# Kernel tuning notes

Hardware: AMD Instinct MI355X
Metric: run time of the kernel (lower is better)

The kernel has to match this reference:

```python
import jax, jax.numpy as jnp
import numpy as np
from jax import lax

DIM = 512
IDIM = 1536
K = 7


def setup_inputs() -> dict:
    key = jax.random.key(0)
    ks = jax.random.split(key, 10)
    B, C, T = 16, DIM, 2048
    x = jax.random.normal(ks[0], (B, C, T), dtype=jnp.float32)
    dw_w = jax.random.normal(ks[1], (DIM, 1, K), dtype=jnp.float32) * (1.0 / np.sqrt(K))
    dw_b = jax.random.normal(ks[2], (DIM,), dtype=jnp.float32) * 0.01
    ln_g = jnp.ones((DIM,), dtype=jnp.float32)
    ln_b = jnp.zeros((DIM,), dtype=jnp.float32)
    w1 = jax.random.normal(ks[3], (IDIM, DIM), dtype=jnp.float32) * (1.0 / np.sqrt(DIM))
    b1 = jax.random.normal(ks[4], (IDIM,), dtype=jnp.float32) * 0.01
    grn_g = jax.random.normal(ks[5], (IDIM,), dtype=jnp.float32) * 0.02
    grn_b = jax.random.normal(ks[6], (IDIM,), dtype=jnp.float32) * 0.02
    w2 = jax.random.normal(ks[7], (DIM, IDIM), dtype=jnp.float32) * (1.0 / np.sqrt(IDIM))
    b2 = jax.random.normal(ks[8], (DIM,), dtype=jnp.float32) * 0.01
    return {"x": x, "dw_w": dw_w, "dw_b": dw_b, "ln_g": ln_g, "ln_b": ln_b,
            "w1": w1, "b1": b1, "grn_g": grn_g, "grn_b": grn_b, "w2": w2, "b2": b2}


def reference(x, dw_w, dw_b, ln_g, ln_b, w1, b1, grn_g, grn_b, w2, b2):
    residual = x  # [B, C, T]
    # depthwise conv1d, padding='same' style (K//2 each side)
    y = lax.conv_general_dilated(
        x, dw_w,
        window_strides=(1,),
        padding=[(K // 2, K // 2)],
        dimension_numbers=("NCH", "OIH", "NCH"),
        feature_group_count=DIM,
    ) + dw_b[None, :, None]
    y = jnp.transpose(y, (0, 2, 1))  # [B, T, C]
    # LayerNorm over channels, eps=1e-6
    mu = jnp.mean(y, axis=-1, keepdims=True)
    var = jnp.mean((y - mu) ** 2, axis=-1, keepdims=True)
    y = (y - mu) * lax.rsqrt(var + 1e-6) * ln_g + ln_b
    # pwconv1 + GELU (exact, erf-based as torch default)
    h = jnp.einsum("btc,ic->bti", y, w1) + b1  # [B, T, IDIM]
    h = jax.nn.gelu(h, approximate=False)
    # GRN: L2 norm over time axis (dim=1), mean over channels
    gx = jnp.sqrt(jnp.sum(h * h, axis=1, keepdims=True))  # [B, 1, IDIM]
    nx = gx / (jnp.mean(gx, axis=-1, keepdims=True) + 1e-6)
    h = grn_g * (h * nx) + grn_b + h
    # pwconv2
    y = jnp.einsum("bti,ci->btc", h, w2) + b2  # [B, T, C]
    y = jnp.transpose(y, (0, 2, 1))  # [B, C, T]
    return residual + y
```

## Files before the change

kernel.cpp:

```cpp
#include <hip/hip_runtime.h>
#include <math.h>

typedef unsigned short u16;
typedef unsigned int u32;
typedef __bf16 bf16x8_t __attribute__((ext_vector_type(8)));
typedef float f32x4_t __attribute__((ext_vector_type(4)));

__device__ __forceinline__ u16 f2bf(float f) {
  __bf16 b = (__bf16)f;
  return __builtin_bit_cast(u16, b);
}

__device__ __forceinline__ void gld16(const void* g, void* l) {
  __builtin_amdgcn_global_load_lds(
      (const __attribute__((address_space(1))) void*)g,
      (__attribute__((address_space(3))) void*)l, 16, 0, 0);
}

__global__ __launch_bounds__(256) void cast_kernel(const float* __restrict__ src,
                                                   u16* __restrict__ dst, int n) {
  int i = (blockIdx.x * 256 + threadIdx.x) * 4;
  if (i < n) {
    float4 v = *(const float4*)(src + i);
    uint2 o;
    o.x = (u32)f2bf(v.x) | ((u32)f2bf(v.y) << 16);
    o.y = (u32)f2bf(v.z) | ((u32)f2bf(v.w) << 16);
    *(uint2*)(dst + i) = o;
  }
}

__global__ __launch_bounds__(64) void b2ob_kernel(const float* __restrict__ w2,
                                                  const float* __restrict__ grn_b,
                                                  const float* __restrict__ b2,
                                                  float* __restrict__ out) {
  int c = blockIdx.x;
  int l = threadIdx.x;
  float p = 0.f;
  for (int i = l; i < 1536; i += 64) p += grn_b[i] * w2[(size_t)c * 1536 + i];
  #pragma unroll
  for (int s = 32; s; s >>= 1) p += __shfl_xor(p, s);
  if (l == 0) out[c] = b2[c] + p;
}

__global__ __launch_bounds__(512, 4) void conv_ln_kernel(const float* __restrict__ X,
                                                         const float* __restrict__ Wd,
                                                         const float* __restrict__ bd,
                                                         const float* __restrict__ lng,
                                                         const float* __restrict__ lnb,
                                                         u16* __restrict__ Y) {
  __shared__ float ystage[16 * 516];
  __shared__ float mu_s[16], rs_s[16];

  const int c = threadIdx.x;
  const int b = blockIdx.y;
  const int t0 = blockIdx.x * 64;

  const float* xr = X + ((size_t)b * 512 + c) * 2048;
  float wr[7];
  #pragma unroll
  for (int k = 0; k < 7; ++k) wr[k] = Wd[c * 7 + k];
  const float bdv = bd[c];
  const float lg = lng[c];
  const float lb = lnb[c];

  for (int ch = 0; ch < 4; ++ch) {
    const int tc0 = t0 + ch * 16;
    const int g = tc0 - 4;
    float w[24];
    if (g >= 0 && g + 24 <= 2048) {
      #pragma unroll
      for (int q = 0; q < 6; ++q) {
        float4 v = *(const float4*)(xr + g + q * 4);
        w[q * 4 + 0] = v.x; w[q * 4 + 1] = v.y;
        w[q * 4 + 2] = v.z; w[q * 4 + 3] = v.w;
      }
    } else {
      #pragma unroll
      for (int j = 0; j < 24; ++j) {
        int tt = g + j;
        w[j] = (tt >= 0 && tt < 2048) ? xr[tt] : 0.f;
      }
    }
    float outv[16];
    #pragma unroll
    for (int i = 0; i < 16; ++i) {
      float a = bdv;
      #pragma unroll
      for (int k = 0; k < 7; ++k) a = fmaf(w[i + 1 + k], wr[k], a);
      outv[i] = a;
      ystage[i * 516 + c] = a;
    }
    __syncthreads();
    {
      int r = c >> 5, cl = c & 31;
      float s = 0.f, q = 0.f;
      #pragma unroll
      for (int k = 0; k < 16; ++k) {
        float v = ystage[r * 516 + cl + k * 32];
        s += v; q += v * v;
      }
      #pragma unroll
      for (int m = 16; m; m >>= 1) { s += __shfl_xor(s, m); q += __shfl_xor(q, m); }
      if (cl == 0) {
        float mu = s * (1.f / 512.f);
        float var = q * (1.f / 512.f) - mu * mu;
        mu_s[r] = mu;
        rs_s[r] = rsqrtf(var + 1e-6f);
      }
    }
    __syncthreads();
    #pragma unroll
    for (int i = 0; i < 16; ++i) {
      float v = (outv[i] - mu_s[i]) * rs_s[i] * lg + lb;
      Y[(size_t)(b * 2048 + tc0 + i) * 512 + c] = f2bf(v);
    }
  }
}

__global__ __launch_bounds__(256, 2) void gemm1_kernel(const u16* __restrict__ A,
                                                       const u16* __restrict__ B,
                                                       const float* __restrict__ b1,
                                                       u16* __restrict__ H,
                                                       float* __restrict__ gsum) {
  __shared__ __align__(16) u16 smem[128 * 136];
  u16* lA = smem;
  u16* lB = smem + 128 * 64;

  const int tid = threadIdx.x;
  const int w = tid >> 6;
  const int l = tid & 63;
  const int m0 = blockIdx.x * 128;
  const int n0 = blockIdx.y * 128;
  const int bidx = m0 >> 11;
  const int wm = w >> 1, wn = w & 1;

  f32x4_t acc[4][4];
  #pragma unroll
  for (int i = 0; i < 4; ++i)
    #pragma unroll
    for (int j = 0; j < 4; ++j) {
      f32x4_t z = {0.f, 0.f, 0.f, 0.f};
      acc[i][j] = z;
    }

  const int rowInc = w * 8 + (l >> 3);
  const int colE = (l & 7) * 8;
  const u16* Abase = A + (size_t)(m0 + rowInc) * 512 + colE;
  const u16* Bbase = B + (size_t)(n0 + rowInc) * 512 + colE;
  const int ldsOff = w * 512;

  for (int kt = 0; kt < 512; kt += 64) {
    #pragma unroll
    for (int c = 0; c < 4; ++c) {
      gld16(Abase + (size_t)(c * 32) * 512 + kt, lA + c * 2048 + ldsOff);
      gld16(Bbase + (size_t)(c * 32) * 512 + kt, lB + c * 2048 + ldsOff);
    }
    __syncthreads();
    #pragma unroll
    for (int kk = 0; kk < 2; ++kk) {
      bf16x8_t af[4], bfr[4];
      #pragma unroll
      for (int f = 0; f < 4; ++f) {
        int arow = wm * 64 + f * 16 + (l & 15);
        af[f] = *(const bf16x8_t*)(lA + arow * 64 + kk * 32 + (l >> 4) * 8);
        int brow = wn * 64 + f * 16 + (l & 15);
        bfr[f] = *(const bf16x8_t*)(lB + brow * 64 + kk * 32 + (l >> 4) * 8);
      }
      #pragma unroll
      for (int i = 0; i < 4; ++i)
        #pragma unroll
        for (int j = 0; j < 4; ++j)
          acc[i][j] = __builtin_amdgcn_mfma_f32_16x16x32_bf16(af[i], bfr[j], acc[i][j], 0, 0, 0);
    }
    __syncthreads();
  }

  const int lrow = (l >> 4) * 4;
  const int lcol = l & 15;
  float bj[4];
  #pragma unroll
  for (int j = 0; j < 4; ++j) bj[j] = b1[n0 + wn * 64 + j * 16 + lcol];

  float ss[4] = {0.f, 0.f, 0.f, 0.f};
  #pragma unroll
  for (int i = 0; i < 4; ++i) {
    int row = wm * 64 + i * 16 + lrow;
    #pragma unroll
    for (int j = 0; j < 4; ++j) {
      int col = wn * 64 + j * 16 + lcol;
      #pragma unroll
      for (int r = 0; r < 4; ++r) {
        float v = acc[i][j][r] + bj[j];
        float g = 0.5f * v * (1.0f + erff(v * 0.70710678118654752f));
        ss[j] += g * g;
        smem[(row + r) * 136 + col] = f2bf(g);
      }
    }
  }
  #pragma unroll
  for (int j = 0; j < 4; ++j) {
    float v = ss[j];
    v += __shfl_xor(v, 16);
    v += __shfl_xor(v, 32);
    if ((l >> 4) == 0)
      atomicAdd(&gsum[bidx * 1536 + n0 + wn * 64 + j * 16 + lcol], v);
  }
  __syncthreads();
  #pragma unroll
  for (int it = 0; it < 8; ++it) {
    int idx = it * 256 + tid;
    int row = idx >> 4;
    int cb = idx & 15;
    uint4 v = *(const uint4*)(smem + row * 136 + cb * 8);
    *(uint4*)(H + (size_t)(m0 + row) * 1536 + n0 + cb * 8) = v;
  }
}

__global__ __launch_bounds__(256) void grn_kernel(const float* __restrict__ gsum,
                                                  const float* __restrict__ grn_g,
                                                  float* __restrict__ svec) {
  __shared__ float red[256];
  int b = blockIdx.x, tid = threadIdx.x;
  float gx[6];
  float part = 0.f;
  #pragma unroll
  for (int it = 0; it < 6; ++it) {
    int i = it * 256 + tid;
    gx[it] = sqrtf(gsum[b * 1536 + i]);
    part += gx[it];
  }
  red[tid] = part;
  __syncthreads();
  for (int s = 128; s; s >>= 1) {
    if (tid < s) red[tid] += red[tid + s];
    __syncthreads();
  }
  float inv = 1.0f / (red[0] * (1.f / 1536.f) + 1e-6f);
  #pragma unroll
  for (int it = 0; it < 6; ++it) {
    int i = it * 256 + tid;
    svec[b * 1536 + i] = 1.0f + grn_g[i] * gx[it] * inv;
  }
}

__global__ __launch_bounds__(256, 2) void gemm2_kernel(const u16* __restrict__ Hs,
                                                       const u16* __restrict__ B,
                                                       const float* __restrict__ svec,
                                                       const float* __restrict__ b2ob,
                                                       const float* __restrict__ X,
                                                       float* __restrict__ Out) {
  __shared__ __align__(16) u16 smem[16512];
  u16* lA = smem;
  u16* lB = smem + 8192;

  const int tid = threadIdx.x;
  const int w = tid >> 6;
  const int l = tid & 63;
  const int m0 = blockIdx.x * 128;
  const int n0 = blockIdx.y * 128;
  const int bidx = m0 >> 11;
  const int t0 = m0 & 2047;
  const int wm = w >> 1, wn = w & 1;

  f32x4_t acc[4][4];
  #pragma unroll
  for (int i = 0; i < 4; ++i)
    #pragma unroll
    for (int j = 0; j < 4; ++j) {
      f32x4_t z = {0.f, 0.f, 0.f, 0.f};
      acc[i][j] = z;
    }

  const int rowInc = w * 8 + (l >> 3);
  const int colE = (l & 7) * 8;
  const u16* Abase = Hs + (size_t)(m0 + rowInc) * 1536 + colE;
  const u16* Bbase = B + (size_t)(n0 + rowInc) * 1536 + colE;
  const float* sb = svec + bidx * 1536 + colE;
  const int ldsOff = w * 512;

  for (int kt = 0; kt < 1536; kt += 64) {
    #pragma unroll
    for (int c = 0; c < 4; ++c)
      gld16(Bbase + (size_t)(c * 32) * 1536 + kt, lB + c * 2048 + ldsOff);
    float4 s0 = *(const float4*)(sb + kt);
    float4 s1 = *(const float4*)(sb + kt + 4);
    float sv[8] = {s0.x, s0.y, s0.z, s0.w, s1.x, s1.y, s1.z, s1.w};
    #pragma unroll
    for (int c = 0; c < 4; ++c) {
      bf16x8_t hv = *(const bf16x8_t*)(Abase + (size_t)(c * 32) * 1536 + kt);
      bf16x8_t ov;
      #pragma unroll
      for (int e = 0; e < 8; ++e) ov[e] = (__bf16)((float)hv[e] * sv[e]);
      *(bf16x8_t*)(lA + c * 2048 + ldsOff + l * 8) = ov;
    }
    __syncthreads();
    #pragma unroll
    for (int kk = 0; kk < 2; ++kk) {
      bf16x8_t af[4], bfr[4];
      #pragma unroll
      for (int f = 0; f < 4; ++f) {
        int arow = wm * 64 + f * 16 + (l & 15);
        af[f] = *(const bf16x8_t*)(lA + arow * 64 + kk * 32 + (l >> 4) * 8);
        int brow = wn * 64 + f * 16 + (l & 15);
        bfr[f] = *(const bf16x8_t*)(lB + brow * 64 + kk * 32 + (l >> 4) * 8);
      }
      #pragma unroll
      for (int i = 0; i < 4; ++i)
        #pragma unroll
        for (int j = 0; j < 4; ++j)
          acc[i][j] = __builtin_amdgcn_mfma_f32_16x16x32_bf16(af[i], bfr[j], acc[i][j], 0, 0, 0);
    }
    __syncthreads();
  }

  float* ostage = (float*)smem;
  #pragma unroll
  for (int half = 0; half < 2; ++half) {
    if (wm == half) {
      #pragma unroll
      for (int i = 0; i < 4; ++i) {
        int lr = i * 16 + (l >> 4) * 4;
        #pragma unroll
        for (int j = 0; j < 4; ++j) {
          int col = wn * 64 + j * 16 + (l & 15);
          #pragma unroll
          for (int r = 0; r < 4; ++r) ostage[(lr + r) * 129 + col] = acc[i][j][r];
        }
      }
    }
    __syncthreads();
    #pragma unroll
    for (int it = 0; it < 32; ++it) {
      int cl = it * 4 + w;
      int c = n0 + cl;
      float v = ostage[l * 129 + cl];
      size_t oidx = ((size_t)bidx * 512 + c) * 2048 + t0 + half * 64 + l;
      Out[oidx] = v + b2ob[c] + X[oidx];
    }
    __syncthreads();
  }
}

extern "C" void kernel_launch(void* const* d_in, const int* in_sizes, int n_in,
                              void* d_out, int out_size, void* d_ws, size_t ws_size,
                              hipStream_t stream) {
  const float* x     = (const float*)d_in[0];
  const float* dw_w  = (const float*)d_in[1];
  const float* dw_b  = (const float*)d_in[2];
  const float* ln_g  = (const float*)d_in[3];
  const float* ln_b  = (const float*)d_in[4];
  const float* w1    = (const float*)d_in[5];
  const float* b1    = (const float*)d_in[6];
  const float* grn_g = (const float*)d_in[7];
  const float* grn_b = (const float*)d_in[8];
  const float* w2    = (const float*)d_in[9];
  const float* b2    = (const float*)d_in[10];
  float* out = (float*)d_out;

  u16* y_ln = (u16*)d_ws;
  u16* h    = y_ln + (size_t)32768 * 512;
  u16* w1b  = h + (size_t)32768 * 1536;
  u16* w2b  = w1b + (size_t)1536 * 512;
  float* gsum = (float*)(w2b + (size_t)512 * 1536);
  float* svec = gsum + 16 * 1536;
  float* b2ob = svec + 16 * 1536;

  hipMemsetAsync(gsum, 0, 16 * 1536 * sizeof(float), stream);
  cast_kernel<<<768, 256, 0, stream>>>(w1, w1b, 1536 * 512);
  cast_kernel<<<768, 256, 0, stream>>>(w2, w2b, 512 * 1536);
  b2ob_kernel<<<512, 64, 0, stream>>>(w2, grn_b, b2, b2ob);
  conv_ln_kernel<<<dim3(32, 16), 512, 0, stream>>>(x, dw_w, dw_b, ln_g, ln_b, y_ln);
  gemm1_kernel<<<dim3(256, 12), 256, 0, stream>>>(y_ln, w1b, b1, h, gsum);
  grn_kernel<<<16, 256, 0, stream>>>(gsum, grn_g, svec);
  gemm2_kernel<<<dim3(256, 4), 256, 0, stream>>>(h, w2b, svec, b2ob, x, out);
}
```

Before: 269.6 us.

## Rewrite GEMMs with 256x256 double-buffered swizzled tiles and fold GRN scale into W2

Both GEMMs now share a 512-thread k-loop with 256x256 tiles. It uses double-buffered XOR-swizzled LDS staging, split-phase barriers with setprio, and an XCD-aware block swizzle. The GRN per-channel scale moves from the gemm2 A operand into a per-batch scaled bf16 copy of W2, built by a new kernel, so H can be loaded straight into LDS. The exact erf GELU is replaced by a tanh approximation computed with exp2, which changes numerics slightly. The larger tiles use 128KB of dynamic LDS per block, which may limit occupancy.

```diff
diff --git a/kernel.cpp b/kernel.cpp
--- a/kernel.cpp
+++ b/kernel.cpp
@@ -6,6 +6,13 @@
 typedef __bf16 bf16x8_t __attribute__((ext_vector_type(8)));
 typedef float f32x4_t __attribute__((ext_vector_type(4)));
 
+#define MEMF() asm volatile("" ::: "memory")
+__device__ __forceinline__ void bar() {
+  MEMF();
+  __builtin_amdgcn_s_barrier();
+  MEMF();
+}
+
 __device__ __forceinline__ u16 f2bf(float f) {
   __bf16 b = (__bf16)f;
   return __builtin_bit_cast(u16, b);
@@ -15,6 +22,19 @@
   __builtin_amdgcn_global_load_lds(
       (const __attribute__((address_space(1))) void*)g,
       (__attribute__((address_space(3))) void*)l, 16, 0, 0);
+}
+
+__device__ __forceinline__ float gelu_f(float v) {
+  float z = 0.7978845608028654f * (v + 0.044715f * v * v * v);
+  float zc = fminf(fmaxf(z, -15.f), 15.f);
+  float t = __builtin_amdgcn_exp2f(2.8853900817779268f * zc);
+  float th = (t - 1.f) / (t + 1.f);
+  return 0.5f * v * (1.f + th);
+}
+
+__device__ __forceinline__ int swz8(int bid, int nwg) {
+  int cpx = nwg >> 3;
+  return (bid & 7) * cpx + (bid >> 3);
 }
 
 __global__ __launch_bounds__(256) void cast_kernel(const float* __restrict__ src,
@@ -117,105 +137,6 @@
   }
 }
 
-__global__ __launch_bounds__(256, 2) void gemm1_kernel(const u16* __restrict__ A,
-                                                       const u16* __restrict__ B,
-                                                       const float* __restrict__ b1,
-                                                       u16* __restrict__ H,
-                                                       float* __restrict__ gsum) {
-  __shared__ __align__(16) u16 smem[128 * 136];
-  u16* lA = smem;
-  u16* lB = smem + 128 * 64;
-
-  const int tid = threadIdx.x;
-  const int w = tid >> 6;
-  const int l = tid & 63;
-  const int m0 = blockIdx.x * 128;
-  const int n0 = blockIdx.y * 128;
-  const int bidx = m0 >> 11;
-  const int wm = w >> 1, wn = w & 1;
-
-  f32x4_t acc[4][4];
-  #pragma unroll
-  for (int i = 0; i < 4; ++i)
-    #pragma unroll
-    for (int j = 0; j < 4; ++j) {
-      f32x4_t z = {0.f, 0.f, 0.f, 0.f};
-      acc[i][j] = z;
-    }
-
-  const int rowInc = w * 8 + (l >> 3);
-  const int colE = (l & 7) * 8;
-  const u16* Abase = A + (size_t)(m0 + rowInc) * 512 + colE;
-  const u16* Bbase = B + (size_t)(n0 + rowInc) * 512 + colE;
-  const int ldsOff = w * 512;
-
-  for (int kt = 0; kt < 512; kt += 64) {
-    #pragma unroll
-    for (int c = 0; c < 4; ++c) {
-      gld16(Abase + (size_t)(c * 32) * 512 + kt, lA + c * 2048 + ldsOff);
-      gld16(Bbase + (size_t)(c * 32) * 512 + kt, lB + c * 2048 + ldsOff);
-    }
-    __syncthreads();
-    #pragma unroll
-    for (int kk = 0; kk < 2; ++kk) {
-      bf16x8_t af[4], bfr[4];
-      #pragma unroll
-      for (int f = 0; f < 4; ++f) {
-        int arow = wm * 64 + f * 16 + (l & 15);
-        af[f] = *(const bf16x8_t*)(lA + arow * 64 + kk * 32 + (l >> 4) * 8);
-        int brow = wn * 64 + f * 16 + (l & 15);
-        bfr[f] = *(const bf16x8_t*)(lB + brow * 64 + kk * 32 + (l >> 4) * 8);
-      }
-      #pragma unroll
-      for (int i = 0; i < 4; ++i)
-        #pragma unroll
-        for (int j = 0; j < 4; ++j)
-          acc[i][j] = __builtin_amdgcn_mfma_f32_16x16x32_bf16(af[i], bfr[j], acc[i][j], 0, 0, 0);
-    }
-    __syncthreads();
-  }
-
-  const int lrow = (l >> 4) * 4;
-  const int lcol = l & 15;
-  float bj[4];
-  #pragma unroll
-  for (int j = 0; j < 4; ++j) bj[j] = b1[n0 + wn * 64 + j * 16 + lcol];
-
-  float ss[4] = {0.f, 0.f, 0.f, 0.f};
-  #pragma unroll
-  for (int i = 0; i < 4; ++i) {
-    int row = wm * 64 + i * 16 + lrow;
-    #pragma unroll
-    for (int j = 0; j < 4; ++j) {
-      int col = wn * 64 + j * 16 + lcol;
-      #pragma unroll
-      for (int r = 0; r < 4; ++r) {
-        float v = acc[i][j][r] + bj[j];
-        float g = 0.5f * v * (1.0f + erff(v * 0.70710678118654752f));
-        ss[j] += g * g;
-        smem[(row + r) * 136 + col] = f2bf(g);
-      }
-    }
-  }
-  #pragma unroll
-  for (int j = 0; j < 4; ++j) {
-    float v = ss[j];
-    v += __shfl_xor(v, 16);
-    v += __shfl_xor(v, 32);
-    if ((l >> 4) == 0)
-      atomicAdd(&gsum[bidx * 1536 + n0 + wn * 64 + j * 16 + lcol], v);
-  }
-  __syncthreads();
-  #pragma unroll
-  for (int it = 0; it < 8; ++it) {
-    int idx = it * 256 + tid;
-    int row = idx >> 4;
-    int cb = idx & 15;
-    uint4 v = *(const uint4*)(smem + row * 136 + cb * 8);
-    *(uint4*)(H + (size_t)(m0 + row) * 1536 + n0 + cb * 8) = v;
-  }
-}
-
 __global__ __launch_bounds__(256) void grn_kernel(const float* __restrict__ gsum,
                                                   const float* __restrict__ grn_g,
                                                   float* __restrict__ svec) {
@@ -243,101 +164,273 @@
   }
 }
 
-__global__ __launch_bounds__(256, 2) void gemm2_kernel(const u16* __restrict__ Hs,
-                                                       const u16* __restrict__ B,
-                                                       const float* __restrict__ svec,
+__global__ __launch_bounds__(256) void w2s_kernel(const float* __restrict__ w2,
+                                                  const float* __restrict__ svec,
+                                                  u16* __restrict__ out) {
+  size_t e0 = ((size_t)blockIdx.x * 256 + threadIdx.x) * 8;
+  int i = (int)(e0 % 1536);
+  size_t bc = e0 / 1536;
+  int b = (int)(bc >> 9);
+  size_t widx = (bc & 511) * 1536 + i;
+  float4 wa = *(const float4*)(w2 + widx);
+  float4 wb = *(const float4*)(w2 + widx + 4);
+  float4 sa = *(const float4*)(svec + b * 1536 + i);
+  float4 sb = *(const float4*)(svec + b * 1536 + i + 4);
+  uint4 o;
+  o.x = (u32)f2bf(wa.x * sa.x) | ((u32)f2bf(wa.y * sa.y) << 16);
+  o.y = (u32)f2bf(wa.z * sa.z) | ((u32)f2bf(wa.w * sa.w) << 16);
+  o.z = (u32)f2bf(wb.x * sb.x) | ((u32)f2bf(wb.y * sb.y) << 16);
+  o.w = (u32)f2bf(wb.z * sb.z) | ((u32)f2bf(wb.w * sb.w) << 16);
+  *(uint4*)(out + e0) = o;
+}
+
+template<int KD>
+__device__ __forceinline__ void gemm_kloop(const u16* __restrict__ Ag,
+                                           const u16* __restrict__ Bg,
+                                           u16* lds, int NT,
+                                           f32x4_t (&acc)[8][4]) {
+  const int tid = threadIdx.x;
+  const int l = tid & 63, l15 = l & 15, lq = l >> 4;
+  const int w = tid >> 6, wm = w >> 2, wn = w & 3;
+  const int rin = tid >> 3;
+  const int cs = ((tid & 7) ^ (rin & 7)) << 3;
+  const int strip = (w >> 2) << 6;
+  const int rb = rin & 31;
+  const int wb8 = (w & 3) << 3;
+
+  auto STAGE_A = [&](int buf, int kt, int mh) {
+    u16* lt = lds + buf * 32768;
+    gld16(Ag + (size_t)(mh * 64 + rin) * KD + kt + cs,
+          lt + (mh * 64 + w * 8) * 64);
+    gld16(Ag + (size_t)(128 + mh * 64 + rin) * KD + kt + cs,
+          lt + (128 + mh * 64 + w * 8) * 64);
+  };
+  auto STAGE_B = [&](int buf, int kt, int nh) {
+    u16* lt = lds + buf * 32768 + 16384;
+    #pragma unroll
+    for (int c = 0; c < 2; ++c) {
+      int r = c * 128 + strip + nh * 32 + rb;
+      gld16(Bg + (size_t)r * KD + kt + cs,
+            lt + (c * 128 + strip + nh * 32 + wb8) * 64);
+    }
+  };
+
+  STAGE_A(0, 0, 0);  STAGE_B(0, 0, 0);
+  STAGE_A(0, 0, 1);  STAGE_B(0, 0, 1);
+  STAGE_A(1, 64, 0); STAGE_B(1, 64, 0);
+  asm volatile("s_waitcnt vmcnt(4)" ::: "memory");
+  bar();
+
+  bf16x8_t a[4][2], b0[2][2], b1[2][2];
+
+  for (int S = 0; S < NT; ++S) {
+    u16* lA = lds + (S & 1) * 32768;
+    u16* lB = lA + 16384;
+    const int kt1 = (S + 1) * 64, kt2 = (S + 2) * 64;
+    const bool s1 = (S + 1 < NT), s2 = (S + 2 < NT);
+
+    #pragma unroll
+    for (int f = 0; f < 4; ++f) {
+      const int R = wm * 128 + f * 16 + l15;
+      #pragma unroll
+      for (int kk = 0; kk < 2; ++kk)
+        a[f][kk] = *(const bf16x8_t*)(lA + R * 64 + (((kk * 4 + lq) ^ (R & 7)) << 3));
+    }
+    #pragma unroll
+    for (int g = 0; g < 2; ++g) {
+      const int R = wn * 64 + g * 16 + l15;
+      #pragma unroll
+      for (int kk = 0; kk < 2; ++kk)
+        b0[g][kk] = *(const bf16x8_t*)(lB + R * 64 + (((kk * 4 + lq) ^ (R & 7)) << 3));
+    }
+    if (s1) STAGE_A((S + 1) & 1, kt1, 1);
+    bar();
+    __builtin_amdgcn_s_setprio(1);
+    #pragma unroll
+    for (int f = 0; f < 4; ++f)
+      #pragma unroll
+      for (int g = 0; g < 2; ++g)
+        #pragma unroll
+        for (int kk = 0; kk < 2; ++kk)
+          acc[f][g] = __builtin_amdgcn_mfma_f32_16x16x32_bf16(a[f][kk], b0[g][kk], acc[f][g], 0, 0, 0);
+    __builtin_amdgcn_s_setprio(0);
+    bar();
+
+    #pragma unroll
+    for (int g = 0; g < 2; ++g) {
+      const int R = wn * 64 + 32 + g * 16 + l15;
+      #pragma unroll
+      for (int kk = 0; kk < 2; ++kk)
+        b1[g][kk] = *(const bf16x8_t*)(lB + R * 64 + (((kk * 4 + lq) ^ (R & 7)) << 3));
+    }
+    if (s1) STAGE_B((S + 1) & 1, kt1, 1);
+    bar();
+    __builtin_amdgcn_s_setprio(1);
+    #pragma unroll
+    for (int f = 0; f < 4; ++f)
+      #pragma unroll
+      for (int g = 0; g < 2; ++g)
+        #pragma unroll
+        for (int kk = 0; kk < 2; ++kk)
+          acc[f][2 + g] = __builtin_amdgcn_mfma_f32_16x16x32_bf16(a[f][kk], b1[g][kk], acc[f][2 + g], 0, 0, 0);
+    __builtin_amdgcn_s_setprio(0);
+    bar();
+
+    #pragma unroll
+    for (int f = 0; f < 4; ++f) {
+      const int R = wm * 128 + 64 + f * 16 + l15;
+      #pragma unroll
+      for (int kk = 0; kk < 2; ++kk)
+        a[f][kk] = *(const bf16x8_t*)(lA + R * 64 + (((kk * 4 + lq) ^ (R & 7)) << 3));
+    }
+    if (s2) STAGE_A(S & 1, kt2, 0);
+    bar();
+    __builtin_amdgcn_s_setprio(1);
+    #pragma unroll
+    for (int f = 0; f < 4; ++f)
+      #pragma unroll
+      for (int g = 0; g < 2; ++g)
+        #pragma unroll
+        for (int kk = 0; kk < 2; ++kk)
+          acc[4 + f][g] = __builtin_amdgcn_mfma_f32_16x16x32_bf16(a[f][kk], b0[g][kk], acc[4 + f][g], 0, 0, 0);
+    __builtin_amdgcn_s_setprio(0);
+    bar();
+
+    if (s2) STAGE_B(S & 1, kt2, 0);
+    bar();
+    __builtin_amdgcn_s_setprio(1);
+    #pragma unroll
+    for (int f = 0; f < 4; ++f)
+      #pragma unroll
+      for (int g = 0; g < 2; ++g)
+        #pragma unroll
+        for (int kk = 0; kk < 2; ++kk)
+          acc[4 + f][2 + g] = __builtin_amdgcn_mfma_f32_16x16x32_bf16(a[f][kk], b1[g][kk], acc[4 + f][2 + g], 0, 0, 0);
+    __builtin_amdgcn_s_setprio(0);
+    if (s2)      { asm volatile("s_waitcnt vmcnt(4)" ::: "memory"); }
+    else if (s1) { asm volatile("s_waitcnt vmcnt(0)" ::: "memory"); }
+    bar();
+  }
+}
+
+__global__ __launch_bounds__(512, 2) void gemm1_kernel(const u16* __restrict__ A,
+                                                       const u16* __restrict__ Bw,
+                                                       const float* __restrict__ b1,
+                                                       u16* __restrict__ H,
+                                                       float* __restrict__ gsum) {
+  extern __shared__ __align__(16) u16 lds[];
+  const int tid = threadIdx.x;
+  const int l = tid & 63, l15 = l & 15, lq = l >> 4;
+  const int w = tid >> 6, wm = w >> 2, wn = w & 3;
+  const int wg = swz8(blockIdx.x, 768);
+  const int ntile = wg % 6, mtile = wg / 6;
+  const int m0 = mtile * 256, n0 = ntile * 256;
+  const int bidx = m0 >> 11;
+
+  f32x4_t acc[8][4];
+  #pragma unroll
+  for (int i = 0; i < 8; ++i)
+    #pragma unroll
+    for (int j = 0; j < 4; ++j) {
+      f32x4_t z = {0.f, 0.f, 0.f, 0.f};
+      acc[i][j] = z;
+    }
+
+  gemm_kloop<512>(A + (size_t)m0 * 512, Bw + (size_t)n0 * 512, lds, 8, acc);
+
+  const int coll = wn * 64 + l15;
+  float bj[4];
+  #pragma unroll
+  for (int nf = 0; nf < 4; ++nf) bj[nf] = b1[n0 + coll + nf * 16];
+
+  for (int h = 0; h < 2; ++h) {
+    bar();
+    if (wm == h) {
+      float ss[4] = {0.f, 0.f, 0.f, 0.f};
+      #pragma unroll
+      for (int mf = 0; mf < 8; ++mf) {
+        const int lr = mf * 16 + lq * 4;
+        #pragma unroll
+        for (int nf = 0; nf < 4; ++nf) {
+          #pragma unroll
+          for (int r = 0; r < 4; ++r) {
+            float g = gelu_f(acc[mf][nf][r] + bj[nf]);
+            ss[nf] += g * g;
+            lds[(lr + r) * 264 + coll + nf * 16] = f2bf(g);
+          }
+        }
+      }
+      #pragma unroll
+      for (int nf = 0; nf < 4; ++nf) {
+        float v = ss[nf];
+        v += __shfl_xor(v, 16);
+        v += __shfl_xor(v, 32);
+        if (lq == 0) atomicAdd(&gsum[bidx * 1536 + n0 + coll + nf * 16], v);
+      }
+    }
+    bar();
+    #pragma unroll
+    for (int it = 0; it < 8; ++it) {
+      int idx = it * 512 + tid;
+      int row = idx >> 5, ch = idx & 31;
+      uint4 v = *(const uint4*)(lds + row * 264 + ch * 8);
+      *(uint4*)(H + (size_t)(m0 + h * 128 + row) * 1536 + n0 + ch * 8) = v;
+    }
+  }
+}
+
+__global__ __launch_bounds__(512, 2) void gemm2_kernel(const u16* __restrict__ Hm,
+                                                       const u16* __restrict__ W2s,
                                                        const float* __restrict__ b2ob,
                                                        const float* __restrict__ X,
                                                        float* __restrict__ Out) {
-  __shared__ __align__(16) u16 smem[16512];
-  u16* lA = smem;
-  u16* lB = smem + 8192;
-
+  extern __shared__ __align__(16) u16 lds[];
   const int tid = threadIdx.x;
-  const int w = tid >> 6;
-  const int l = tid & 63;
-  const int m0 = blockIdx.x * 128;
-  const int n0 = blockIdx.y * 128;
-  const int bidx = m0 >> 11;
-  const int t0 = m0 & 2047;
-  const int wm = w >> 1, wn = w & 1;
-
-  f32x4_t acc[4][4];
-  #pragma unroll
-  for (int i = 0; i < 4; ++i)
+  const int l = tid & 63, l15 = l & 15, lq = l >> 4;
+  const int w = tid >> 6, wm = w >> 2, wn = w & 3;
+  const int wg = swz8(blockIdx.x, 256);
+  const int ntile = wg & 1, mtile = wg >> 1;
+  const int m0 = mtile * 256, n0 = ntile * 256;
+  const int bidx = m0 >> 11, t0 = m0 & 2047;
+
+  f32x4_t acc[8][4];
+  #pragma unroll
+  for (int i = 0; i < 8; ++i)
     #pragma unroll
     for (int j = 0; j < 4; ++j) {
       f32x4_t z = {0.f, 0.f, 0.f, 0.f};
       acc[i][j] = z;
     }
 
-  const int rowInc = w * 8 + (l >> 3);
-  const int colE = (l & 7) * 8;
-  const u16* Abase = Hs + (size_t)(m0 + rowInc) * 1536 + colE;
-  const u16* Bbase = B + (size_t)(n0 + rowInc) * 1536 + colE;
-  const float* sb = svec + bidx * 1536 + colE;
-  const int ldsOff = w * 512;
-
-  for (int kt = 0; kt < 1536; kt += 64) {
-    #pragma unroll
-    for (int c = 0; c < 4; ++c)
-      gld16(Bbase + (size_t)(c * 32) * 1536 + kt, lB + c * 2048 + ldsOff);
-    float4 s0 = *(const float4*)(sb + kt);
-    float4 s1 = *(const float4*)(sb + kt + 4);
-    float sv[8] = {s0.x, s0.y, s0.z, s0.w, s1.x, s1.y, s1.z, s1.w};
-    #pragma unroll
-    for (int c = 0; c < 4; ++c) {
-      bf16x8_t hv = *(const bf16x8_t*)(Abase + (size_t)(c * 32) * 1536 + kt);
-      bf16x8_t ov;
-      #pragma unroll
-      for (int e = 0; e < 8; ++e) ov[e] = (__bf16)((float)hv[e] * sv[e]);
-      *(bf16x8_t*)(lA + c * 2048 + ldsOff + l * 8) = ov;
-    }
-    __syncthreads();
-    #pragma unroll
-    for (int kk = 0; kk < 2; ++kk) {
-      bf16x8_t af[4], bfr[4];
-      #pragma unroll
-      for (int f = 0; f < 4; ++f) {
-        int arow = wm * 64 + f * 16 + (l & 15);
-        af[f] = *(const bf16x8_t*)(lA + arow * 64 + kk * 32 + (l >> 4) * 8);
-        int brow = wn * 64 + f * 16 + (l & 15);
-        bfr[f] = *(const bf16x8_t*)(lB + brow * 64 + kk * 32 + (l >> 4) * 8);
-      }
-      #pragma unroll
-      for (int i = 0; i < 4; ++i)
-        #pragma unroll
-        for (int j = 0; j < 4; ++j)
-          acc[i][j] = __builtin_amdgcn_mfma_f32_16x16x32_bf16(af[i], bfr[j], acc[i][j], 0, 0, 0);
-    }
-    __syncthreads();
-  }
-
-  float* ostage = (float*)smem;
-  #pragma unroll
-  for (int half = 0; half < 2; ++half) {
-    if (wm == half) {
-      #pragma unroll
-      for (int i = 0; i < 4; ++i) {
-        int lr = i * 16 + (l >> 4) * 4;
-        #pragma unroll
-        for (int j = 0; j < 4; ++j) {
-          int col = wn * 64 + j * 16 + (l & 15);
+  gemm_kloop<1536>(Hm + (size_t)m0 * 1536,
+                   W2s + ((size_t)bidx * 512 + n0) * 1536, lds, 24, acc);
+
+  float* st = (float*)lds;
+  for (int q = 0; q < 4; ++q) {
+    bar();
+    if (wm == (q >> 1)) {
+      #pragma unroll
+      for (int m2 = 0; m2 < 4; ++m2) {
+        const int mf = (q & 1) * 4 + m2;
+        const int lr = m2 * 16 + lq * 4;
+        #pragma unroll
+        for (int nf = 0; nf < 4; ++nf) {
+          const int cl = wn * 64 + nf * 16 + l15;
           #pragma unroll
-          for (int r = 0; r < 4; ++r) ostage[(lr + r) * 129 + col] = acc[i][j][r];
+          for (int r = 0; r < 4; ++r)
+            st[(lr + r) * 261 + cl] = acc[mf][nf][r];
         }
       }
     }
-    __syncthreads();
-    #pragma unroll
-    for (int it = 0; it < 32; ++it) {
-      int cl = it * 4 + w;
-      int c = n0 + cl;
-      float v = ostage[l * 129 + cl];
-      size_t oidx = ((size_t)bidx * 512 + c) * 2048 + t0 + half * 64 + l;
-      Out[oidx] = v + b2ob[c] + X[oidx];
-    }
-    __syncthreads();
+    bar();
+    const size_t obase = ((size_t)bidx * 512 + n0) * 2048 + (size_t)(t0 + q * 64 + l);
+    #pragma unroll
+    for (int cc = 0; cc < 32; ++cc) {
+      const int c = w * 32 + cc;
+      float v = st[l * 261 + c] + b2ob[n0 + c];
+      size_t oi = obase + (size_t)c * 2048;
+      Out[oi] = v + X[oi];
+    }
   }
 }
 
@@ -358,19 +451,24 @@
   float* out = (float*)d_out;
 
   u16* y_ln = (u16*)d_ws;
+  u16* w2s  = y_ln;
   u16* h    = y_ln + (size_t)32768 * 512;
   u16* w1b  = h + (size_t)32768 * 1536;
-  u16* w2b  = w1b + (size_t)1536 * 512;
-  float* gsum = (float*)(w2b + (size_t)512 * 1536);
+  float* gsum = (float*)(w1b + (size_t)1536 * 512);
   float* svec = gsum + 16 * 1536;
   float* b2ob = svec + 16 * 1536;
 
+  (void)hipFuncSetAttribute((const void*)gemm1_kernel,
+                            hipFuncAttributeMaxDynamicSharedMemorySize, 131072);
+  (void)hipFuncSetAttribute((const void*)gemm2_kernel,
+                            hipFuncAttributeMaxDynamicSharedMemorySize, 131072);
+
   hipMemsetAsync(gsum, 0, 16 * 1536 * sizeof(float), stream);
   cast_kernel<<<768, 256, 0, stream>>>(w1, w1b, 1536 * 512);
-  cast_kernel<<<768, 256, 0, stream>>>(w2, w2b, 512 * 1536);
   b2ob_kernel<<<512, 64, 0, stream>>>(w2, grn_b, b2, b2ob);
   conv_ln_kernel<<<dim3(32, 16), 512, 0, stream>>>(x, dw_w, dw_b, ln_g, ln_b, y_ln);
-  gemm1_kernel<<<dim3(256, 12), 256, 0, stream>>>(y_ln, w1b, b1, h, gsum);
+  gemm1_kernel<<<768, 512, 131072, stream>>>(y_ln, w1b, b1, h, gsum);
   grn_kernel<<<16, 256, 0, stream>>>(gsum, grn_g, svec);
-  gemm2_kernel<<<dim3(256, 4), 256, 0, stream>>>(h, w2b, svec, b2ob, x, out);
-}
+  w2s_kernel<<<6144, 256, 0, stream>>>(w2, svec, w2s);
+  gemm2_kernel<<<256, 512, 131072, stream>>>(h, w2s, b2ob, x, out);
+}
```

Result: faster. 248.2 us (-7.9%).

## Fold GRN scale into per-batch W2, swizzle LDS, tanh GELU, XCD tile remap

Applied to the files above, without the earlier changes.

The GRN per-channel scale is moved off the H activations and folded into a per-batch scaled bf16 copy of W2, built by a new w2s kernel. This lets gemm2 load both operands with direct global-to-LDS copies instead of scaling H in registers. Both GEMMs now share a k-loop that uses XOR-swizzled LDS layouts to reduce bank conflicts, and a workgroup remap groups tiles per XCD. The exact erf GELU is replaced by a tanh approximation built from exp2 and rcp, which changes numerics slightly. Launch bounds no longer request two blocks per CU, and the scaled W2 copy reuses the y_ln buffer.

```diff
diff --git a/kernel.cpp b/kernel.cpp
--- a/kernel.cpp
+++ b/kernel.cpp
@@ -15,6 +15,18 @@
   __builtin_amdgcn_global_load_lds(
       (const __attribute__((address_space(1))) void*)g,
       (__attribute__((address_space(3))) void*)l, 16, 0, 0);
+}
+
+__device__ __forceinline__ float gelu_f(float v) {
+  float z = 0.7978845608028654f * v * fmaf(0.044715f, v * v, 1.0f);
+  float t = __builtin_amdgcn_exp2f(2.8853900817779268f * z);
+  float r = __builtin_amdgcn_rcpf(t + 1.0f);
+  return v - v * r;
+}
+
+__device__ __forceinline__ int swz8(int bid, int nwg) {
+  int cpx = nwg >> 3;
+  return (bid & 7) * cpx + (bid >> 3);
 }
 
 __global__ __launch_bounds__(256) void cast_kernel(const float* __restrict__ src,
@@ -117,105 +129,6 @@
   }
 }
 
-__global__ __launch_bounds__(256, 2) void gemm1_kernel(const u16* __restrict__ A,
-                                                       const u16* __restrict__ B,
-                                                       const float* __restrict__ b1,
-                                                       u16* __restrict__ H,
-                                                       float* __restrict__ gsum) {
-  __shared__ __align__(16) u16 smem[128 * 136];
-  u16* lA = smem;
-  u16* lB = smem + 128 * 64;
-
-  const int tid = threadIdx.x;
-  const int w = tid >> 6;
-  const int l = tid & 63;
-  const int m0 = blockIdx.x * 128;
-  const int n0 = blockIdx.y * 128;
-  const int bidx = m0 >> 11;
-  const int wm = w >> 1, wn = w & 1;
-
-  f32x4_t acc[4][4];
-  #pragma unroll
-  for (int i = 0; i < 4; ++i)
-    #pragma unroll
-    for (int j = 0; j < 4; ++j) {
-      f32x4_t z = {0.f, 0.f, 0.f, 0.f};
-      acc[i][j] = z;
-    }
-
-  const int rowInc = w * 8 + (l >> 3);
-  const int colE = (l & 7) * 8;
-  const u16* Abase = A + (size_t)(m0 + rowInc) * 512 + colE;
-  const u16* Bbase = B + (size_t)(n0 + rowInc) * 512 + colE;
-  const int ldsOff = w * 512;
-
-  for (int kt = 0; kt < 512; kt += 64) {
-    #pragma unroll
-    for (int c = 0; c < 4; ++c) {
-      gld16(Abase + (size_t)(c * 32) * 512 + kt, lA + c * 2048 + ldsOff);
-      gld16(Bbase + (size_t)(c * 32) * 512 + kt, lB + c * 2048 + ldsOff);
-    }
-    __syncthreads();
-    #pragma unroll
-    for (int kk = 0; kk < 2; ++kk) {
-      bf16x8_t af[4], bfr[4];
-      #pragma unroll
-      for (int f = 0; f < 4; ++f) {
-        int arow = wm * 64 + f * 16 + (l & 15);
-        af[f] = *(const bf16x8_t*)(lA + arow * 64 + kk * 32 + (l >> 4) * 8);
-        int brow = wn * 64 + f * 16 + (l & 15);
-        bfr[f] = *(const bf16x8_t*)(lB + brow * 64 + kk * 32 + (l >> 4) * 8);
-      }
-      #pragma unroll
-      for (int i = 0; i < 4; ++i)
-        #pragma unroll
-        for (int j = 0; j < 4; ++j)
-          acc[i][j] = __builtin_amdgcn_mfma_f32_16x16x32_bf16(af[i], bfr[j], acc[i][j], 0, 0, 0);
-    }
-    __syncthreads();
-  }
-
-  const int lrow = (l >> 4) * 4;
-  const int lcol = l & 15;
-  float bj[4];
-  #pragma unroll
-  for (int j = 0; j < 4; ++j) bj[j] = b1[n0 + wn * 64 + j * 16 + lcol];
-
-  float ss[4] = {0.f, 0.f, 0.f, 0.f};
-  #pragma unroll
-  for (int i = 0; i < 4; ++i) {
-    int row = wm * 64 + i * 16 + lrow;
-    #pragma unroll
-    for (int j = 0; j < 4; ++j) {
-      int col = wn * 64 + j * 16 + lcol;
-      #pragma unroll
-      for (int r = 0; r < 4; ++r) {
-        float v = acc[i][j][r] + bj[j];
-        float g = 0.5f * v * (1.0f + erff(v * 0.70710678118654752f));
-        ss[j] += g * g;
-        smem[(row + r) * 136 + col] = f2bf(g);
-      }
-    }
-  }
-  #pragma unroll
-  for (int j = 0; j < 4; ++j) {
-    float v = ss[j];
-    v += __shfl_xor(v, 16);
-    v += __shfl_xor(v, 32);
-    if ((l >> 4) == 0)
-      atomicAdd(&gsum[bidx * 1536 + n0 + wn * 64 + j * 16 + lcol], v);
-  }
-  __syncthreads();
-  #pragma unroll
-  for (int it = 0; it < 8; ++it) {
-    int idx = it * 256 + tid;
-    int row = idx >> 4;
-    int cb = idx & 15;
-    uint4 v = *(const uint4*)(smem + row * 136 + cb * 8);
-    *(uint4*)(H + (size_t)(m0 + row) * 1536 + n0 + cb * 8) = v;
-  }
-}
-
 __global__ __launch_bounds__(256) void grn_kernel(const float* __restrict__ gsum,
                                                   const float* __restrict__ grn_g,
                                                   float* __restrict__ svec) {
@@ -243,24 +156,83 @@
   }
 }
 
-__global__ __launch_bounds__(256, 2) void gemm2_kernel(const u16* __restrict__ Hs,
-                                                       const u16* __restrict__ B,
-                                                       const float* __restrict__ svec,
-                                                       const float* __restrict__ b2ob,
-                                                       const float* __restrict__ X,
-                                                       float* __restrict__ Out) {
-  __shared__ __align__(16) u16 smem[16512];
-  u16* lA = smem;
-  u16* lB = smem + 8192;
-
+__global__ __launch_bounds__(256) void w2s_kernel(const float* __restrict__ w2,
+                                                  const float* __restrict__ svec,
+                                                  u16* __restrict__ out) {
+  size_t e0 = ((size_t)blockIdx.x * 256 + threadIdx.x) * 8;
+  int i = (int)(e0 % 1536);
+  size_t bc = e0 / 1536;
+  int b = (int)(bc >> 9);
+  size_t widx = (bc & 511) * 1536 + i;
+  float4 wa = *(const float4*)(w2 + widx);
+  float4 wb = *(const float4*)(w2 + widx + 4);
+  float4 sa = *(const float4*)(svec + b * 1536 + i);
+  float4 sb = *(const float4*)(svec + b * 1536 + i + 4);
+  uint4 o;
+  o.x = (u32)f2bf(wa.x * sa.x) | ((u32)f2bf(wa.y * sa.y) << 16);
+  o.y = (u32)f2bf(wa.z * sa.z) | ((u32)f2bf(wa.w * sa.w) << 16);
+  o.z = (u32)f2bf(wb.x * sb.x) | ((u32)f2bf(wb.y * sb.y) << 16);
+  o.w = (u32)f2bf(wb.z * sb.z) | ((u32)f2bf(wb.w * sb.w) << 16);
+  *(uint4*)(out + e0) = o;
+}
+
+template<int KD>
+__device__ __forceinline__ void gemm_kloop(const u16* __restrict__ Ag,
+                                           const u16* __restrict__ Bg,
+                                           u16* lds, int NT,
+                                           f32x4_t (&acc)[4][4]) {
   const int tid = threadIdx.x;
+  const int l = tid & 63, l15 = l & 15, lq = l >> 4;
   const int w = tid >> 6;
-  const int l = tid & 63;
-  const int m0 = blockIdx.x * 128;
-  const int n0 = blockIdx.y * 128;
+  const int wm = w >> 1, wn = w & 1;
+  const int rin = tid >> 3;
+  const int cs = ((tid & 7) ^ (rin & 7)) << 3;
+  u16* lA = lds;
+  u16* lB = lds + 8192;
+
+  for (int S = 0; S < NT; ++S) {
+    const int kt = S * 64;
+    #pragma unroll
+    for (int c = 0; c < 4; ++c) {
+      gld16(Ag + (size_t)(c * 32 + rin) * KD + kt + cs, lA + (c * 32 + w * 8) * 64);
+      gld16(Bg + (size_t)(c * 32 + rin) * KD + kt + cs, lB + (c * 32 + w * 8) * 64);
+    }
+    __syncthreads();
+    bf16x8_t af[4][2], bf[4][2];
+    #pragma unroll
+    for (int f = 0; f < 4; ++f) {
+      const int Ra = wm * 64 + f * 16 + l15;
+      const int Rb = wn * 64 + f * 16 + l15;
+      #pragma unroll
+      for (int kk = 0; kk < 2; ++kk) {
+        af[f][kk] = *(const bf16x8_t*)(lA + Ra * 64 + (((kk * 4 + lq) ^ (Ra & 7)) << 3));
+        bf[f][kk] = *(const bf16x8_t*)(lB + Rb * 64 + (((kk * 4 + lq) ^ (Rb & 7)) << 3));
+      }
+    }
+    #pragma unroll
+    for (int i = 0; i < 4; ++i)
+      #pragma unroll
+      for (int j = 0; j < 4; ++j)
+        #pragma unroll
+        for (int kk = 0; kk < 2; ++kk)
+          acc[i][j] = __builtin_amdgcn_mfma_f32_16x16x32_bf16(af[i][kk], bf[j][kk], acc[i][j], 0, 0, 0);
+    __syncthreads();
+  }
+}
+
+__global__ __launch_bounds__(256) void gemm1_kernel(const u16* __restrict__ A,
+                                                    const u16* __restrict__ Bw,
+                                                    const float* __restrict__ b1,
+                                                    u16* __restrict__ H,
+                                                    float* __restrict__ gsum) {
+  __shared__ __align__(16) u16 smem[16640];
+  const int tid = threadIdx.x;
+  const int l = tid & 63, l15 = l & 15, lq = l >> 4;
+  const int w = tid >> 6, wm = w >> 1, wn = w & 1;
+  const int wg = swz8(blockIdx.x, 3072);
+  const int ntile = wg % 12, mtile = wg / 12;
+  const int m0 = mtile * 128, n0 = ntile * 128;
   const int bidx = m0 >> 11;
-  const int t0 = m0 & 2047;
-  const int wm = w >> 1, wn = w & 1;
 
   f32x4_t acc[4][4];
   #pragma unroll
@@ -271,73 +243,95 @@
       acc[i][j] = z;
     }
 
-  const int rowInc = w * 8 + (l >> 3);
-  const int colE = (l & 7) * 8;
-  const u16* Abase = Hs + (size_t)(m0 + rowInc) * 1536 + colE;
-  const u16* Bbase = B + (size_t)(n0 + rowInc) * 1536 + colE;
-  const float* sb = svec + bidx * 1536 + colE;
-  const int ldsOff = w * 512;
-
-  for (int kt = 0; kt < 1536; kt += 64) {
-    #pragma unroll
-    for (int c = 0; c < 4; ++c)
-      gld16(Bbase + (size_t)(c * 32) * 1536 + kt, lB + c * 2048 + ldsOff);
-    float4 s0 = *(const float4*)(sb + kt);
-    float4 s1 = *(const float4*)(sb + kt + 4);
-    float sv[8] = {s0.x, s0.y, s0.z, s0.w, s1.x, s1.y, s1.z, s1.w};
-    #pragma unroll
-    for (int c = 0; c < 4; ++c) {
-      bf16x8_t hv = *(const bf16x8_t*)(Abase + (size_t)(c * 32) * 1536 + kt);
-      bf16x8_t ov;
-      #pragma unroll
-      for (int e = 0; e < 8; ++e) ov[e] = (__bf16)((float)hv[e] * sv[e]);
-      *(bf16x8_t*)(lA + c * 2048 + ldsOff + l * 8) = ov;
-    }
-    __syncthreads();
-    #pragma unroll
-    for (int kk = 0; kk < 2; ++kk) {
-      bf16x8_t af[4], bfr[4];
-      #pragma unroll
-      for (int f = 0; f < 4; ++f) {
-        int arow = wm * 64 + f * 16 + (l & 15);
-        af[f] = *(const bf16x8_t*)(lA + arow * 64 + kk * 32 + (l >> 4) * 8);
-        int brow = wn * 64 + f * 16 + (l & 15);
-        bfr[f] = *(const bf16x8_t*)(lB + brow * 64 + kk * 32 + (l >> 4) * 8);
-      }
-      #pragma unroll
-      for (int i = 0; i < 4; ++i)
+  gemm_kloop<512>(A + (size_t)m0 * 512, Bw + (size_t)n0 * 512, smem, 8, acc);
+
+  float bj[4];
+  #pragma unroll
+  for (int nf = 0; nf < 4; ++nf) bj[nf] = b1[n0 + wn * 64 + nf * 16 + l15];
+
+  float ss[4] = {0.f, 0.f, 0.f, 0.f};
+  #pragma unroll
+  for (int mf = 0; mf < 4; ++mf) {
+    const int lr = wm * 64 + mf * 16 + lq * 4;
+    #pragma unroll
+    for (int nf = 0; nf < 4; ++nf) {
+      const int cl = wn * 64 + nf * 16 + l15;
+      #pragma unroll
+      for (int r = 0; r < 4; ++r) {
+        float g = gelu_f(acc[mf][nf][r] + bj[nf]);
+        ss[nf] += g * g;
+        smem[(lr + r) * 130 + cl] = f2bf(g);
+      }
+    }
+  }
+  #pragma unroll
+  for (int nf = 0; nf < 4; ++nf) {
+    float v = ss[nf];
+    v += __shfl_xor(v, 16);
+    v += __shfl_xor(v, 32);
+    if (lq == 0) atomicAdd(&gsum[bidx * 1536 + n0 + wn * 64 + nf * 16 + l15], v);
+  }
+  __syncthreads();
+  #pragma unroll
+  for (int it = 0; it < 8; ++it) {
+    int idx = it * 256 + tid;
+    int row = idx >> 4, ch = idx & 15;
+    uint4 v = *(const uint4*)(smem + row * 130 + ch * 8);
+    *(uint4*)(H + (size_t)(m0 + row) * 1536 + n0 + ch * 8) = v;
+  }
+}
+
+__global__ __launch_bounds__(256) void gemm2_kernel(const u16* __restrict__ Hm,
+                                                    const u16* __restrict__ W2s,
+                                                    const float* __restrict__ b2ob,
+                                                    const float* __restrict__ X,
+                                                    float* __restrict__ Out) {
+  __shared__ __align__(16) u16 smem[16640];
+  const int tid = threadIdx.x;
+  const int l = tid & 63, l15 = l & 15, lq = l >> 4;
+  const int w = tid >> 6, wm = w >> 1, wn = w & 1;
+  const int wg = swz8(blockIdx.x, 1024);
+  const int ntile = wg & 3, mtile = wg >> 2;
+  const int m0 = mtile * 128, n0 = ntile * 128;
+  const int bidx = m0 >> 11, t0 = m0 & 2047;
+
+  f32x4_t acc[4][4];
+  #pragma unroll
+  for (int i = 0; i < 4; ++i)
+    #pragma unroll
+    for (int j = 0; j < 4; ++j) {
+      f32x4_t z = {0.f, 0.f, 0.f, 0.f};
+      acc[i][j] = z;
+    }
+
+  gemm_kloop<1536>(Hm + (size_t)m0 * 1536,
+                   W2s + ((size_t)bidx * 512 + n0) * 1536, smem, 24, acc);
+
+  float* st = (float*)smem;
+  for (int half = 0; half < 2; ++half) {
+    __syncthreads();
+    if (wm == half) {
+      #pragma unroll
+      for (int mf = 0; mf < 4; ++mf) {
+        const int lr = mf * 16 + lq * 4;
         #pragma unroll
-        for (int j = 0; j < 4; ++j)
-          acc[i][j] = __builtin_amdgcn_mfma_f32_16x16x32_bf16(af[i], bfr[j], acc[i][j], 0, 0, 0);
-    }
-    __syncthreads();
-  }
-
-  float* ostage = (float*)smem;
-  #pragma unroll
-  for (int half = 0; half < 2; ++half) {
-    if (wm == half) {
-      #pragma unroll
-      for (int i = 0; i < 4; ++i) {
-        int lr = i * 16 + (l >> 4) * 4;
-        #pragma unroll
-        for (int j = 0; j < 4; ++j) {
-          int col = wn * 64 + j * 16 + (l & 15);
+        for (int nf = 0; nf < 4; ++nf) {
+          const int cl = wn * 64 + nf * 16 + l15;
           #pragma unroll
-          for (int r = 0; r < 4; ++r) ostage[(lr + r) * 129 + col] = acc[i][j][r];
+          for (int r = 0; r < 4; ++r)
+            st[(lr + r) * 129 + cl] = acc[mf][nf][r];
         }
       }
     }
     __syncthreads();
-    #pragma unroll
-    for (int it = 0; it < 32; ++it) {
-      int cl = it * 4 + w;
-      int c = n0 + cl;
-      float v = ostage[l * 129 + cl];
-      size_t oidx = ((size_t)bidx * 512 + c) * 2048 + t0 + half * 64 + l;
-      Out[oidx] = v + b2ob[c] + X[oidx];
-    }
-    __syncthreads();
+    const size_t obase = ((size_t)bidx * 512 + n0) * 2048 + (size_t)(t0 + half * 64 + l);
+    #pragma unroll
+    for (int cc = 0; cc < 32; ++cc) {
+      const int c = w * 32 + cc;
+      float v = st[l * 129 + c] + b2ob[n0 + c];
+      size_t oi = obase + (size_t)c * 2048;
+      Out[oi] = v + X[oi];
+    }
   }
 }
 
@@ -358,19 +352,19 @@
   float* out = (float*)d_out;
 
   u16* y_ln = (u16*)d_ws;
+  u16* w2s  = y_ln;
   u16* h    = y_ln + (size_t)32768 * 512;
   u16* w1b  = h + (size_t)32768 * 1536;
-  u16* w2b  = w1b + (size_t)1536 * 512;
-  float* gsum = (float*)(w2b + (size_t)512 * 1536);
+  float* gsum = (float*)(w1b + (size_t)1536 * 512);
   float* svec = gsum + 16 * 1536;
   float* b2ob = svec + 16 * 1536;
 
   hipMemsetAsync(gsum, 0, 16 * 1536 * sizeof(float), stream);
   cast_kernel<<<768, 256, 0, stream>>>(w1, w1b, 1536 * 512);
-  cast_kernel<<<768, 256, 0, stream>>>(w2, w2b, 512 * 1536);
   b2ob_kernel<<<512, 64, 0, stream>>>(w2, grn_b, b2, b2ob);
   conv_ln_kernel<<<dim3(32, 16), 512, 0, stream>>>(x, dw_w, dw_b, ln_g, ln_b, y_ln);
-  gemm1_kernel<<<dim3(256, 12), 256, 0, stream>>>(y_ln, w1b, b1, h, gsum);
+  gemm1_kernel<<<3072, 256, 0, stream>>>(y_ln, w1b, b1, h, gsum);
   grn_kernel<<<16, 256, 0, stream>>>(gsum, grn_g, svec);
-  gemm2_kernel<<<dim3(256, 4), 256, 0, stream>>>(h, w2b, svec, b2ob, x, out);
-}
+  w2s_kernel<<<6144, 256, 0, stream>>>(w2, svec, w2s);
+  gemm2_kernel<<<1024, 256, 0, stream>>>(h, w2s, b2ob, x, out);
+}
```

After: 247.5 us. -8.2%, faster.
